# Performance work log

Hardware: AMD Instinct MI355X
Metric: run time of the kernel (lower is better)

The kernel has to match this reference:

```python
import jax, jax.numpy as jnp
import numpy as np

N, E, IN, HID, OUT, HEADS = 50000, 400000, 32, 400, 4, 1


def setup_inputs() -> dict:
    key = jax.random.key(0)
    ks = jax.random.split(key, 11)
    x = jax.random.normal(ks[0], (N, IN), dtype=jnp.float32)
    src = jax.random.randint(ks[1], (E,), 0, N)
    dst = jax.random.randint(ks[2], (E,), 0, N)
    edge_index = jnp.stack([src, dst]).astype(jnp.int64)
    W1 = jax.random.normal(ks[3], (IN, HEADS * HID), dtype=jnp.float32) * (1.0 / np.sqrt(IN))
    u1 = jax.random.normal(ks[4], (IN, HEADS), dtype=jnp.float32) * (1.0 / np.sqrt(IN))
    c1 = jax.random.normal(ks[5], (HEADS,), dtype=jnp.float32)
    b1 = jax.random.normal(ks[6], (HID,), dtype=jnp.float32) * 0.02
    W2 = jax.random.normal(ks[7], (HID, HEADS * OUT), dtype=jnp.float32) * (1.0 / np.sqrt(HID))
    u2 = jax.random.normal(ks[8], (HID, HEADS), dtype=jnp.float32) * (1.0 / np.sqrt(HID))
    c2 = jax.random.normal(ks[9], (HEADS,), dtype=jnp.float32)
    b2 = jax.random.normal(ks[10], (OUT,), dtype=jnp.float32) * 0.02
    return {"x": x, "edge_index": edge_index, "W1": W1, "u1": u1, "c1": c1,
            "b1": b1, "W2": W2, "u2": u2, "c2": c2, "b2": b2}


def _feast(h, src, dst, deg, W, u, c, b):
    # PyG FeaStConv: q_h = softmax_h(u^T (x_j - x_i) + c), mean-aggregated.
    heads = u.shape[1]
    out_ch = W.shape[1] // heads
    q = jax.nn.softmax(h[src] @ u - h[dst] @ u + c, axis=-1)      # [E, H]
    m = (h[src] @ W).reshape(-1, heads, out_ch)                   # [E, H, C]
    m = (m * q[..., None]).sum(axis=1)                            # [E, C]
    agg = jax.ops.segment_sum(m, dst, num_segments=h.shape[0]) / deg[:, None]
    return agg + b


def reference(x, edge_index, W1, u1, c1, b1, W2, u2, c2, b2):
    n = x.shape[0]
    loops = jnp.arange(n, dtype=edge_index.dtype)
    src = jnp.concatenate([edge_index[0], loops])   # add_self_loops=True
    dst = jnp.concatenate([edge_index[1], loops])
    deg = jax.ops.segment_sum(jnp.ones_like(dst, jnp.float32), dst, num_segments=n)
    h = jax.nn.relu(_feast(x, src, dst, deg, W1, u1, c1, b1))
    # dropout(p=0.1) is identity in eval mode
    h = jax.nn.relu(_feast(h, src, dst, deg, W2, u2, c2, b2))
    return h
```

## Files before the change

kernel.cpp:

```cpp
#include <hip/hip_runtime.h>


#define TPB 256
#define CAP 32

typedef __attribute__((ext_vector_type(8))) short bf16x8;
typedef __attribute__((ext_vector_type(4))) float f32x4;

__device__ __forceinline__ void split_bf16(float f, ushort& hi, ushort& lo) {
    unsigned u = __float_as_uint(f);
    unsigned h = u >> 16;
    float fh = __uint_as_float(h << 16);
    float r = f - fh;
    hi = (ushort)h;
    lo = (ushort)(__float_as_uint(r) >> 16);
}

__global__ void k_prep(int* __restrict__ cnt, int n1, int zb,
                       const float* __restrict__ W1,
                       ushort* __restrict__ packHi, ushort* __restrict__ packLo) {
    if ((int)blockIdx.x < zb) {
        int gid = blockIdx.x * TPB + threadIdx.x;
        if (gid < n1) cnt[gid] = 0;
    } else {
        int t = (blockIdx.x - zb) * TPB + threadIdx.x;
        if (t >= 25 * 64) return;
        int ct = t >> 6, l = t & 63;
        int kh = l >> 4, c = l & 15;
#pragma unroll
        for (int e = 0; e < 8; e++) {
            float f = W1[(8 * kh + e) * 400 + ct * 16 + c];
            ushort h, lo; split_bf16(f, h, lo);
            packHi[t * 8 + e] = h;
            packLo[t * 8 + e] = lo;
        }
    }
}

__global__ void k_fill(const int* __restrict__ src, const int* __restrict__ dst,
                       int* __restrict__ cnt, int* __restrict__ bucket,
                       int* __restrict__ ovf_cnt, int2* __restrict__ ovf_list, int E) {
    int e = blockIdx.x * TPB + threadIdx.x;
    if (e >= E) return;
    int d = dst[e];
    int s = src[e];
    int slot = atomicAdd(&cnt[d], 1);
    if (slot < CAP) bucket[(size_t)d * CAP + slot] = s;
    else { int pos = atomicAdd(ovf_cnt, 1); ovf_list[pos] = make_int2(s, d); }
}

__global__ __launch_bounds__(256) void k_gdense(
    const float* __restrict__ x, const int* __restrict__ cnt,
    const int* __restrict__ bucket, const int* __restrict__ ovf_cnt,
    const int2* __restrict__ ovf_list,
    const ushort* __restrict__ packHi, const ushort* __restrict__ packLo,
    const float* __restrict__ b1, const float* __restrict__ W2,
    float* __restrict__ p, int n) {
    __shared__ float lb1[400];
    __shared__ __align__(16) float lW2[1600];
    for (int i = threadIdx.x; i < 400; i += 256) lb1[i] = b1[i];
    for (int i = threadIdx.x; i < 1600; i += 256) lW2[i] = W2[i];

    int wid = threadIdx.x >> 6, l = threadIdx.x & 63;
    int base_w = blockIdx.x * 64 + wid * 16;
    int r = l & 15, kh = l >> 4;

    int node = base_w + r; if (node > n - 1) node = n - 1;
    int m = cnt[node];
    int mb = m < CAP ? m : CAP;

    const float4* xp = (const float4*)(x + (size_t)node * 32 + kh * 8);
    float4 s0 = xp[0], s1 = xp[1];
    float acc[8] = {s0.x, s0.y, s0.z, s0.w, s1.x, s1.y, s1.z, s1.w};

    const int4* bkt = (const int4*)(bucket + (size_t)node * CAP);
#pragma unroll
    for (int c4 = 0; c4 < CAP / 4; c4++) {
        if (4 * c4 < mb) {
            int4 b = bkt[c4];
            int base_s = 4 * c4;
            int ids[4] = {b.x, b.y, b.z, b.w};
#pragma unroll
            for (int j = 0; j < 4; j++) {
                if (base_s + j < mb) {
                    const float4* vp = (const float4*)(x + (size_t)ids[j] * 32 + kh * 8);
                    float4 v0 = vp[0], v1 = vp[1];
                    acc[0] += v0.x; acc[1] += v0.y; acc[2] += v0.z; acc[3] += v0.w;
                    acc[4] += v1.x; acc[5] += v1.y; acc[6] += v1.z; acc[7] += v1.w;
                }
            }
        }
    }
    if (m > CAP) {
        int L = ovf_cnt[0];
        for (int j = 0; j < L; j++) {
            int2 sd = ovf_list[j];
            if (sd.y == node) {
                const float4* vp = (const float4*)(x + (size_t)sd.x * 32 + kh * 8);
                float4 v0 = vp[0], v1 = vp[1];
                acc[0] += v0.x; acc[1] += v0.y; acc[2] += v0.z; acc[3] += v0.w;
                acc[4] += v1.x; acc[5] += v1.y; acc[6] += v1.z; acc[7] += v1.w;
            }
        }
    }

    bf16x8 a_hi, a_lo;
#pragma unroll
    for (int e = 0; e < 8; e++) {
        ushort h, lo; split_bf16(acc[e], h, lo);
        a_hi[e] = (short)h; a_lo[e] = (short)lo;
    }

    float invd_q[4];
#pragma unroll
    for (int q = 0; q < 4; q++) {
        int nq = base_w + kh * 4 + q; if (nq > n - 1) nq = n - 1;
        invd_q[q] = 1.0f / (float)(cnt[nq] + 1);
    }

    __syncthreads();

    float pacc[4][4];
#pragma unroll
    for (int q = 0; q < 4; q++)
#pragma unroll
        for (int o = 0; o < 4; o++) pacc[q][o] = 0.f;

    for (int ct = 0; ct < 25; ct++) {
        bf16x8 bh = *(const bf16x8*)(packHi + ((size_t)ct * 64 + l) * 8);
        bf16x8 bl = *(const bf16x8*)(packLo + ((size_t)ct * 64 + l) * 8);
        f32x4 c = {0.f, 0.f, 0.f, 0.f};
        c = __builtin_amdgcn_mfma_f32_16x16x32_bf16(a_hi, bh, c, 0, 0, 0);
        c = __builtin_amdgcn_mfma_f32_16x16x32_bf16(a_lo, bh, c, 0, 0, 0);
        c = __builtin_amdgcn_mfma_f32_16x16x32_bf16(a_hi, bl, c, 0, 0, 0);
        float b1v = lb1[ct * 16 + r];
        const float4 w2v = *(const float4*)(&lW2[(ct * 16 + r) * 4]);
#pragma unroll
        for (int q = 0; q < 4; q++) {
            float h = fmaxf(fmaf(c[q], invd_q[q], b1v), 0.f);
            pacc[q][0] = fmaf(h, w2v.x, pacc[q][0]);
            pacc[q][1] = fmaf(h, w2v.y, pacc[q][1]);
            pacc[q][2] = fmaf(h, w2v.z, pacc[q][2]);
            pacc[q][3] = fmaf(h, w2v.w, pacc[q][3]);
        }
    }
#pragma unroll
    for (int mask = 1; mask <= 8; mask <<= 1)
#pragma unroll
        for (int q = 0; q < 4; q++)
#pragma unroll
            for (int o = 0; o < 4; o++)
                pacc[q][o] += __shfl_xor(pacc[q][o], mask, 64);

    if (r < 4) {
        int nd = base_w + kh * 4 + r;
        if (nd < n)
            *(float4*)(p + (size_t)nd * 4) =
                make_float4(pacc[r][0], pacc[r][1], pacc[r][2], pacc[r][3]);
    }
}

__global__ void k_out(const float* __restrict__ p, const int* __restrict__ cnt,
                      const int* __restrict__ bucket, const int* __restrict__ ovf_cnt,
                      const int2* __restrict__ ovf_list,
                      const float* __restrict__ b2, float* __restrict__ out, int n) {
    int gid = blockIdx.x * blockDim.x + threadIdx.x;
    int node = gid >> 2, c = gid & 3;
    if (node >= n) return;
    int m = cnt[node];
    int mb = m < CAP ? m : CAP;
    float acc = p[(size_t)node * 4 + c];
    const int4* bkt = (const int4*)(bucket + (size_t)node * CAP);
#pragma unroll
    for (int c4 = 0; c4 < CAP / 4; c4++) {
        if (4 * c4 < mb) {
            int4 b = bkt[c4];
            int base_s = 4 * c4;
            int ids[4] = {b.x, b.y, b.z, b.w};
#pragma unroll
            for (int j = 0; j < 4; j++) {
                if (base_s + j < mb) acc += p[(size_t)ids[j] * 4 + c];
            }
        }
    }
    if (m > CAP) {
        int L = ovf_cnt[0];
        for (int j = 0; j < L; j++) {
            int2 sd = ovf_list[j];
            if (sd.y == node) acc += p[(size_t)sd.x * 4 + c];
        }
    }
    out[gid] = fmaxf(fmaf(acc, 1.0f / (float)(m + 1), b2[c]), 0.f);
}

static inline size_t align4i(size_t v) { return (v + 3) & ~(size_t)3; }

extern "C" void kernel_launch(void* const* d_in, const int* in_sizes, int n_in,
                              void* d_out, int out_size, void* d_ws, size_t ws_size,
                              hipStream_t stream) {
    const float* x  = (const float*)d_in[0];
    const int*   ei = (const int*)d_in[1];
    const float* W1 = (const float*)d_in[2];
    const float* b1 = (const float*)d_in[5];
    const float* W2 = (const float*)d_in[6];
    const float* b2 = (const float*)d_in[9];

    int n = in_sizes[0] / 32;
    int E = in_sizes[1] / 2;
    const int* src = ei;
    const int* dst = ei + E;

    int* wsi = (int*)d_ws;
    size_t off = 0;
    int* cnt      = wsi + off; off += n;
    int* ovf_cnt  = wsi + off; off += 1;
    size_t off_ovf = align4i(off);
    int2* ovf_list = (int2*)(wsi + off_ovf); off = off_ovf + 2 * (size_t)E;
    size_t off_b  = align4i(off);
    int* bucket   = wsi + off_b;  off = off_b + (size_t)n * CAP;
    size_t off_p  = align4i(off);
    float* p      = (float*)(wsi + off_p); off = off_p + (size_t)n * 4;
    size_t off_ph = align4i(off);
    ushort* packHi = (ushort*)(wsi + off_ph); off = off_ph + 25 * 64 * 8 / 2;
    ushort* packLo = (ushort*)(wsi + off);
    float* out    = (float*)d_out;

    int zb = (n + 1 + TPB - 1) / TPB;
    k_prep<<<zb + 7, TPB, 0, stream>>>(cnt, n + 1, zb, W1, packHi, packLo);
    k_fill<<<(E + TPB - 1) / TPB, TPB, 0, stream>>>(src, dst, cnt, bucket,
                                                    ovf_cnt, ovf_list, E);
    k_gdense<<<(n + 63) / 64, 256, 0, stream>>>(x, cnt, bucket, ovf_cnt, ovf_list,
                                                packHi, packLo, b1, W2, p, n);
    k_out<<<((size_t)n * 4 + TPB - 1) / TPB, TPB, 0, stream>>>(p, cnt, bucket,
                                                               ovf_cnt, ovf_list,
                                                               b2, out, n);
}
```

Measured before the change: 71.41 us.

## Pack W1 bf16 splits in shared memory per block, drop prep kernel, shrink bucket cap

Removes the separate k_prep kernel: each k_gdense block now converts W1 into hi/lo bf16 fragments in shared memory (about 51 KB), and the counter array is zeroed with hipMemsetAsync. b1 and W2 are read straight from global memory instead of being staged in LDS. The bucket capacity drops from 32 to 16, so more high-degree nodes go through the linear overflow scan. Each block now redoes the W1 split, and the larger LDS footprint may lower occupancy.

```diff
diff --git a/kernel.cpp b/kernel.cpp
--- a/kernel.cpp
+++ b/kernel.cpp
@@ -2,7 +2,7 @@
 
 
 #define TPB 256
-#define CAP 32
+#define CAP 16
 
 typedef __attribute__((ext_vector_type(8))) short bf16x8;
 typedef __attribute__((ext_vector_type(4))) float f32x4;
@@ -14,27 +14,6 @@
     float r = f - fh;
     hi = (ushort)h;
     lo = (ushort)(__float_as_uint(r) >> 16);
-}
-
-__global__ void k_prep(int* __restrict__ cnt, int n1, int zb,
-                       const float* __restrict__ W1,
-                       ushort* __restrict__ packHi, ushort* __restrict__ packLo) {
-    if ((int)blockIdx.x < zb) {
-        int gid = blockIdx.x * TPB + threadIdx.x;
-        if (gid < n1) cnt[gid] = 0;
-    } else {
-        int t = (blockIdx.x - zb) * TPB + threadIdx.x;
-        if (t >= 25 * 64) return;
-        int ct = t >> 6, l = t & 63;
-        int kh = l >> 4, c = l & 15;
-#pragma unroll
-        for (int e = 0; e < 8; e++) {
-            float f = W1[(8 * kh + e) * 400 + ct * 16 + c];
-            ushort h, lo; split_bf16(f, h, lo);
-            packHi[t * 8 + e] = h;
-            packLo[t * 8 + e] = lo;
-        }
-    }
 }
 
 __global__ void k_fill(const int* __restrict__ src, const int* __restrict__ dst,
@@ -52,14 +31,23 @@
 __global__ __launch_bounds__(256) void k_gdense(
     const float* __restrict__ x, const int* __restrict__ cnt,
     const int* __restrict__ bucket, const int* __restrict__ ovf_cnt,
-    const int2* __restrict__ ovf_list,
-    const ushort* __restrict__ packHi, const ushort* __restrict__ packLo,
+    const int2* __restrict__ ovf_list, const float* __restrict__ W1,
     const float* __restrict__ b1, const float* __restrict__ W2,
     float* __restrict__ p, int n) {
-    __shared__ float lb1[400];
-    __shared__ __align__(16) float lW2[1600];
-    for (int i = threadIdx.x; i < 400; i += 256) lb1[i] = b1[i];
-    for (int i = threadIdx.x; i < 1600; i += 256) lW2[i] = W2[i];
+    __shared__ __align__(16) ushort sHi[12800];
+    __shared__ __align__(16) ushort sLo[12800];
+
+    for (int pair = threadIdx.x; pair < 1600; pair += TPB) {
+        int ct = pair >> 6, l = pair & 63;
+        int kh = l >> 4, c = l & 15;
+#pragma unroll
+        for (int e = 0; e < 8; e++) {
+            float f = W1[(8 * kh + e) * 400 + ct * 16 + c];
+            ushort h, lo; split_bf16(f, h, lo);
+            sHi[pair * 8 + e] = h;
+            sLo[pair * 8 + e] = lo;
+        }
+    }
 
     int wid = threadIdx.x >> 6, l = threadIdx.x & 63;
     int base_w = blockIdx.x * 64 + wid * 16;
@@ -127,14 +115,14 @@
         for (int o = 0; o < 4; o++) pacc[q][o] = 0.f;
 
     for (int ct = 0; ct < 25; ct++) {
-        bf16x8 bh = *(const bf16x8*)(packHi + ((size_t)ct * 64 + l) * 8);
-        bf16x8 bl = *(const bf16x8*)(packLo + ((size_t)ct * 64 + l) * 8);
+        bf16x8 bh = *(const bf16x8*)(sHi + ((ct * 64 + l) << 3));
+        bf16x8 bl = *(const bf16x8*)(sLo + ((ct * 64 + l) << 3));
         f32x4 c = {0.f, 0.f, 0.f, 0.f};
         c = __builtin_amdgcn_mfma_f32_16x16x32_bf16(a_hi, bh, c, 0, 0, 0);
         c = __builtin_amdgcn_mfma_f32_16x16x32_bf16(a_lo, bh, c, 0, 0, 0);
         c = __builtin_amdgcn_mfma_f32_16x16x32_bf16(a_hi, bl, c, 0, 0, 0);
-        float b1v = lb1[ct * 16 + r];
-        const float4 w2v = *(const float4*)(&lW2[(ct * 16 + r) * 4]);
+        float b1v = b1[ct * 16 + r];
+        const float4 w2v = *(const float4*)(W2 + (size_t)(ct * 16 + r) * 4);
 #pragma unroll
         for (int q = 0; q < 4; q++) {
             float h = fmaxf(fmaf(c[q], invd_q[q], b1v), 0.f);
@@ -219,18 +207,14 @@
     size_t off_b  = align4i(off);
     int* bucket   = wsi + off_b;  off = off_b + (size_t)n * CAP;
     size_t off_p  = align4i(off);
-    float* p      = (float*)(wsi + off_p); off = off_p + (size_t)n * 4;
-    size_t off_ph = align4i(off);
-    ushort* packHi = (ushort*)(wsi + off_ph); off = off_ph + 25 * 64 * 8 / 2;
-    ushort* packLo = (ushort*)(wsi + off);
+    float* p      = (float*)(wsi + off_p);
     float* out    = (float*)d_out;
 
-    int zb = (n + 1 + TPB - 1) / TPB;
-    k_prep<<<zb + 7, TPB, 0, stream>>>(cnt, n + 1, zb, W1, packHi, packLo);
+    hipMemsetAsync(cnt, 0, (size_t)(n + 1) * sizeof(int), stream);
     k_fill<<<(E + TPB - 1) / TPB, TPB, 0, stream>>>(src, dst, cnt, bucket,
                                                     ovf_cnt, ovf_list, E);
     k_gdense<<<(n + 63) / 64, 256, 0, stream>>>(x, cnt, bucket, ovf_cnt, ovf_list,
-                                                packHi, packLo, b1, W2, p, n);
+                                                W1, b1, W2, p, n);
     k_out<<<((size_t)n * 4 + TPB - 1) / TPB, TPB, 0, stream>>>(p, cnt, bucket,
                                                                ovf_cnt, ovf_list,
                                                                b2, out, n);
```

Measured after the change: 113.2 us. 58.5% more time.
